# Performance work log

Measured on AMD Instinct MI355X. Metric: run time of the kernel, lower is better.

## Reference

```python
import jax, jax.numpy as jnp
import numpy as np

USER_NUM = 100000
ITEM_NUM = 200000
N_NODES = USER_NUM + ITEM_NUM
EMB_DIM = 64
NNZ = 2000000
BATCH = 4096
NODE_DROP = 0.1
MSG_DROP = 0.1
DECAY = 1e-4
NEG_SLOPE = 0.2
EPS = 1e-12


def setup_inputs() -> dict:
    key = jax.random.key(0)
    ks = jax.random.split(key, 24)
    inp = {
        'edge_row': jax.random.randint(ks[0], (NNZ,), 0, N_NODES, dtype=jnp.int32),
        'edge_col': jax.random.randint(ks[1], (NNZ,), 0, N_NODES, dtype=jnp.int32),
        'edge_vals': jax.random.uniform(ks[2], (NNZ,), dtype=jnp.float32),
        'user_emb': jax.random.normal(ks[3], (USER_NUM, EMB_DIM), dtype=jnp.float32) * 0.1,
        'item_emb': jax.random.normal(ks[4], (ITEM_NUM, EMB_DIM), dtype=jnp.float32) * 0.1,
        'user_id': jax.random.randint(ks[5], (BATCH,), 0, USER_NUM, dtype=jnp.int32),
        'item_id': jax.random.randint(ks[6], (BATCH,), 0, ITEM_NUM, dtype=jnp.int32),
        'neg_item_id': jax.random.randint(ks[7], (BATCH,), 0, ITEM_NUM, dtype=jnp.int32),
    }
    scale = 1.0 / np.sqrt(EMB_DIM)
    for k in range(3):
        inp['W_gc_%d' % k] = jax.random.normal(ks[8 + 4 * k], (EMB_DIM, EMB_DIM), dtype=jnp.float32) * scale
        inp['b_gc_%d' % k] = jax.random.normal(ks[9 + 4 * k], (1, EMB_DIM), dtype=jnp.float32) * 0.01
        inp['W_bi_%d' % k] = jax.random.normal(ks[10 + 4 * k], (EMB_DIM, EMB_DIM), dtype=jnp.float32) * scale
        inp['b_bi_%d' % k] = jax.random.normal(ks[11 + 4 * k], (1, EMB_DIM), dtype=jnp.float32) * 0.01
    return inp


def _ngcf_loss(edge_row, edge_col, edge_vals, user_emb, item_emb, layer_params,
               user_id, item_id, neg_item_id):
    # Deterministic dropout masks (fixed key) -> reproducible reference.
    key = jax.random.key(42)
    k_node, k_msg = jax.random.split(key)

    # Sparse (node) dropout on adjacency values, rescaled by 1/keep.
    keep_e = 1.0 - NODE_DROP
    emask = jax.random.bernoulli(k_node, keep_e, edge_vals.shape)
    vals = jnp.where(emask, edge_vals, 0.0) * (1.0 / keep_e)

    ego = jnp.concatenate([user_emb, item_emb], axis=0)  # [N, D]
    all_embs = [ego]
    keep_m = 1.0 - MSG_DROP
    for k, (Wg, bg, Wb, bb) in enumerate(layer_params):
        # SpMM: side[i] = sum_j A[i,j] * ego[j]  (irregular gather + segment_sum)
        gathered = vals[:, None] * ego[edge_col]          # [nnz, D]
        side = jax.ops.segment_sum(gathered, edge_row, num_segments=N_NODES)
        sum_emb = side @ Wg + bg                          # graph-conv transform
        bi_emb = (ego * side) @ Wb + bb                   # bi-interaction transform
        ego = jax.nn.leaky_relu(sum_emb + bi_emb, NEG_SLOPE)
        mmask = jax.random.bernoulli(jax.random.fold_in(k_msg, k), keep_m, ego.shape)
        ego = jnp.where(mmask, ego, 0.0) * (1.0 / keep_m)  # message dropout
        norm = jnp.sqrt(jnp.sum(ego * ego, axis=1, keepdims=True))
        all_embs.append(ego / jnp.maximum(norm, EPS))      # L2 normalize per node
    all_emb = jnp.concatenate(all_embs, axis=1)           # [N, 4*D]
    u_g = all_emb[:USER_NUM]
    i_g = all_emb[USER_NUM:]

    users = u_g[user_id]
    pos = i_g[item_id]
    neg = i_g[neg_item_id]
    pos_s = jnp.sum(users * pos, axis=1)
    neg_s = jnp.sum(users * neg, axis=1)
    mf_loss = -jnp.mean(jax.nn.log_sigmoid(pos_s - neg_s))
    reg = (jnp.sum(users ** 2) + jnp.sum(pos ** 2) + jnp.sum(neg ** 2)) * 0.5
    emb_loss = DECAY * reg / BATCH
    return mf_loss + emb_loss, mf_loss, emb_loss


def reference(edge_row, edge_col, edge_vals, user_emb, item_emb,
              W_gc_0, b_gc_0, W_bi_0, b_bi_0,
              W_gc_1, b_gc_1, W_bi_1, b_bi_1,
              W_gc_2, b_gc_2, W_bi_2, b_bi_2,
              user_id, item_id, neg_item_id):
    layer_params = [(W_gc_0, b_gc_0, W_bi_0, b_bi_0),
                    (W_gc_1, b_gc_1, W_bi_1, b_bi_1),
                    (W_gc_2, b_gc_2, W_bi_2, b_bi_2)]
    loss, mf_loss, emb_loss = _ngcf_loss(edge_row, edge_col, edge_vals,
                                         user_emb, item_emb, layer_params,
                                         user_id, item_id, neg_item_id)
    return loss, mf_loss, emb_loss
```

## Files before the change

kernel.cpp:

```cpp
#include <hip/hip_runtime.h>
#include <stdint.h>

#define USER_NUM 100000
#define ITEM_NUM 200000
#define N_NODES  300000
#define EMB      64
#define NNZ      2000000
#define BATCH    4096
#define R1M      1000000u
#define HALF_MSG 9600000u
#define HALF_N   150000
#define INVK     1.1111111111111112f

#define NBK2     256
#define BROWS    1172
#define BCAP2    7680
#define ABLK     480
#define ACH      4167
#define LDSCAP   3968

typedef short short8 __attribute__((ext_vector_type(8)));
typedef float f32x4  __attribute__((ext_vector_type(4)));

__host__ __device__ inline uint32_t rotl32(uint32_t v, int r) {
    return (v << r) | (v >> (32 - r));
}

__host__ __device__ inline void threefry2x32(uint32_t k0, uint32_t k1,
                                             uint32_t x0, uint32_t x1,
                                             uint32_t& o0, uint32_t& o1) {
    uint32_t k2 = k0 ^ k1 ^ 0x1BD11BDAu;
    x0 += k0; x1 += k1;
#define TF_R(r) { x0 += x1; x1 = rotl32(x1, r); x1 ^= x0; }
    TF_R(13) TF_R(15) TF_R(26) TF_R(6)
    x0 += k1; x1 += k2 + 1u;
    TF_R(17) TF_R(29) TF_R(16) TF_R(24)
    x0 += k2; x1 += k0 + 2u;
    TF_R(13) TF_R(15) TF_R(26) TF_R(6)
    x0 += k0; x1 += k1 + 3u;
    TF_R(17) TF_R(29) TF_R(16) TF_R(24)
    x0 += k1; x1 += k2 + 4u;
    TF_R(13) TF_R(15) TF_R(26) TF_R(6)
    x0 += k2; x1 += k0 + 5u;
#undef TF_R
    o0 = x0; o1 = x1;
}

__host__ __device__ inline float tf_uniform(uint32_t bits) {
    uint32_t fb = (bits >> 9) | 0x3f800000u;
    return __builtin_bit_cast(float, fb) - 1.0f;
}

__device__ inline float bf2f(uint16_t u) {
    uint32_t x = ((uint32_t)u) << 16;
    return __builtin_bit_cast(float, x);
}
__device__ inline uint16_t f2bf(float f) {
    uint32_t x = __builtin_bit_cast(uint32_t, f);
    uint32_t r = (x + 0x7FFFu + ((x >> 16) & 1u)) >> 16;
    return (uint16_t)r;
}

__global__ __launch_bounds__(256) void k_conv(const float* __restrict__ u,
                                              const float* __restrict__ it,
                                              uint16_t* __restrict__ dst) {
    int i = blockIdx.x * 256 + threadIdx.x;
    const int TOT = N_NODES * EMB / 4;
    if (i >= TOT) return;
    const int UQ = USER_NUM * EMB / 4;
    float4 f = (i < UQ) ? ((const float4*)u)[i] : ((const float4*)it)[i - UQ];
    ushort4 o;
    o.x = f2bf(f.x); o.y = f2bf(f.y); o.z = f2bf(f.z); o.w = f2bf(f.w);
    ((ushort4*)dst)[i] = o;
}

__global__ __launch_bounds__(256) void k_sortA(const int* __restrict__ erow,
                                               const int* __restrict__ ecol,
                                               const float* __restrict__ evals,
                                               uint32_t* __restrict__ bcnt,
                                               uint2* __restrict__ tmp,
                                               uint32_t kn0, uint32_t kn1) {
    __shared__ uint32_t hist[NBK2];
    __shared__ uint32_t lstart[NBK2];
    __shared__ uint32_t gbase[NBK2];
    __shared__ uint32_t cur[NBK2];
    __shared__ uint32_t eidx[LDSCAP];
    __shared__ uint8_t  keepb[ACH];
    int tid = threadIdx.x;
    int base = blockIdx.x * ACH;
    int lim = min(ACH, NNZ - base);
    hist[tid] = 0u;
    __syncthreads();
    for (int j = tid; j < lim; j += 256) {
        uint32_t e = (uint32_t)(base + j);
        uint32_t x0 = (e < R1M) ? e : e - R1M;
        uint32_t o0, o1;
        threefry2x32(kn0, kn1, x0, x0 + R1M, o0, o1);
        uint32_t bits = (e < R1M) ? o0 : o1;
        bool kp = tf_uniform(bits) < 0.9f;
        keepb[j] = kp ? 1u : 0u;
        if (kp) atomicAdd(&hist[(uint32_t)erow[e] / BROWS], 1u);
    }
    __syncthreads();
    uint32_t x = hist[tid];
    lstart[tid] = x;
    __syncthreads();
    for (int off = 1; off < 256; off <<= 1) {
        uint32_t y = (tid >= off) ? lstart[tid - off] : 0u;
        __syncthreads();
        lstart[tid] += y;
        __syncthreads();
    }
    uint32_t exc = lstart[tid] - x;
    uint32_t gb = 0u;
    if (x) gb = atomicAdd(&bcnt[tid], x);
    lstart[tid] = exc;
    gbase[tid] = gb;
    cur[tid] = exc;
    __syncthreads();
    for (int j = tid; j < lim; j += 256) {
        if (keepb[j]) {
            uint32_t e = (uint32_t)(base + j);
            uint32_t b = (uint32_t)erow[e] / BROWS;
            uint32_t p = atomicAdd(&cur[b], 1u);
            if (p < LDSCAP) eidx[p] = e;
        }
    }
    __syncthreads();
    uint32_t total = min(lstart[NBK2 - 1] + hist[NBK2 - 1], (uint32_t)LDSCAP);
    for (uint32_t p = tid; p < total; p += 256) {
        uint32_t e = eidx[p];
        uint32_t row = (uint32_t)erow[e];
        uint32_t b = row / BROWS;
        uint32_t off = gbase[b] + (p - lstart[b]);
        if (off < BCAP2) {
            uint2 q;
            q.x = (uint32_t)ecol[e] | ((row - b * BROWS) << 19);
            q.y = __builtin_bit_cast(uint32_t, evals[e] * INVK);
            tmp[(size_t)b * BCAP2 + off] = q;
        }
    }
}

__global__ __launch_bounds__(256) void k_sortB(const uint2* __restrict__ tmp,
                                               const uint32_t* __restrict__ bcnt,
                                               uint2* __restrict__ cv,
                                               uint32_t* __restrict__ rowstart,
                                               uint32_t* __restrict__ rowend) {
    __shared__ uint32_t hist[1280];
    __shared__ uint32_t tsum[256];
    int b = blockIdx.x;
    int t = threadIdx.x;
    uint32_t cnt = min(bcnt[b], (uint32_t)BCAP2);
    for (int i = t; i < 1280; i += 256) hist[i] = 0u;
    __syncthreads();
    const uint2* src = tmp + (size_t)b * BCAP2;
    for (uint32_t i = t; i < cnt; i += 256)
        atomicAdd(&hist[src[i].x >> 19], 1u);
    __syncthreads();
    uint32_t l[5];
    uint32_t s = 0u;
#pragma unroll
    for (int i = 0; i < 5; ++i) { l[i] = hist[t * 5 + i]; s += l[i]; }
    tsum[t] = s;
    __syncthreads();
    for (int off = 1; off < 256; off <<= 1) {
        uint32_t y = (t >= off) ? tsum[t - off] : 0u;
        __syncthreads();
        tsum[t] += y;
        __syncthreads();
    }
    uint32_t run = tsum[t] - s;
    uint32_t cvb = (uint32_t)b * BCAP2;
#pragma unroll
    for (int i = 0; i < 5; ++i) {
        uint32_t e0 = run;
        run += l[i];
        int idx = t * 5 + i;
        int row = b * BROWS + idx;
        if (idx < BROWS && row < N_NODES) {
            rowstart[row] = cvb + e0;
            rowend[row]   = cvb + run;
        }
        hist[idx] = e0;
    }
    __syncthreads();
    for (uint32_t i = t; i < cnt; i += 256) {
        uint2 p = src[i];
        uint32_t rl = p.x >> 19;
        uint32_t pos = atomicAdd(&hist[rl], 1u);
        uint2 q;
        q.x = p.x & 0x7FFFFu;
        q.y = p.y;
        cv[(size_t)cvb + pos] = q;
    }
}

__global__ __launch_bounds__(256) void k_spmv(const uint16_t* __restrict__ ego,
                                              uint16_t* __restrict__ side,
                                              const uint32_t* __restrict__ rowstart,
                                              const uint32_t* __restrict__ rowend,
                                              const uint2* __restrict__ cv) {
    int lane = threadIdx.x & 63;
    int wv = __builtin_amdgcn_readfirstlane((int)((blockIdx.x * 256 + threadIdx.x) >> 6));
    int nw = (gridDim.x * 256) >> 6;
    for (int n0 = wv * 2; n0 < N_NODES; n0 += nw * 2) {
        uint32_t st  = __builtin_amdgcn_readfirstlane(rowstart[n0]);
        uint32_t mid = __builtin_amdgcn_readfirstlane(rowend[n0]);
        uint32_t en  = __builtin_amdgcn_readfirstlane(rowend[n0 + 1]);
        float acc0 = 0.0f, acc1 = 0.0f;
        for (uint32_t j0 = st; j0 < en; j0 += 8) {
            uint32_t cx[8];
            float v0[8], v1[8];
#pragma unroll
            for (int u = 0; u < 8; ++u) {
                uint2 p = cv[j0 + u];
                uint32_t idx = j0 + (uint32_t)u;
                bool ok = idx < en;
                bool r1 = idx >= mid;
                cx[u] = ok ? p.x : 0u;
                float v = ok ? __builtin_bit_cast(float, p.y) : 0.0f;
                v0[u] = r1 ? 0.0f : v;
                v1[u] = r1 ? v : 0.0f;
            }
            float g[8];
#pragma unroll
            for (int u = 0; u < 8; ++u)
                g[u] = bf2f(ego[(size_t)cx[u] * 64 + lane]);
#pragma unroll
            for (int u = 0; u < 8; ++u) {
                acc0 = fmaf(v0[u], g[u], acc0);
                acc1 = fmaf(v1[u], g[u], acc1);
            }
        }
        side[(size_t)n0 * 64 + lane] = f2bf(acc0);
        side[(size_t)(n0 + 1) * 64 + lane] = f2bf(acc1);
    }
}

__device__ inline short8 mul_frag(short8 s, uint4 e) {
    uint32_t ew[4] = {e.x, e.y, e.z, e.w};
    short8 r;
#pragma unroll
    for (int i = 0; i < 4; ++i) {
        float a0 = bf2f((uint16_t)s[2 * i])     * bf2f((uint16_t)(ew[i] & 0xffffu));
        float a1 = bf2f((uint16_t)s[2 * i + 1]) * bf2f((uint16_t)(ew[i] >> 16));
        r[2 * i]     = (short)f2bf(a0);
        r[2 * i + 1] = (short)f2bf(a1);
    }
    return r;
}

__global__ __launch_bounds__(256) void k_dense_mfma(
        uint16_t* __restrict__ ego, const uint16_t* __restrict__ side,
        const float* __restrict__ Wg, const float* __restrict__ bg,
        const float* __restrict__ Wb, const float* __restrict__ bb,
        uint32_t km0, uint32_t km1) {
    int lane = threadIdx.x & 63;
    int wave = (blockIdx.x * 256 + threadIdx.x) >> 6;
    int nw = (gridDim.x * 256) >> 6;
    int m = lane & 15;
    int g = lane >> 4;

    short8 bfr[4][4];
#pragma unroll
    for (int kk = 0; kk < 4; ++kk) {
        const float* W = (kk < 2) ? Wg : Wb;
        int krow = (kk & 1) * 32 + 8 * g;
#pragma unroll
        for (int nt = 0; nt < 4; ++nt) {
#pragma unroll
            for (int i = 0; i < 8; ++i)
                bfr[kk][nt][i] = (short)f2bf(W[(krow + i) * 64 + 16 * nt + m]);
        }
    }
    float bias[4];
#pragma unroll
    for (int nt = 0; nt < 4; ++nt)
        bias[nt] = bg[16 * nt + m] + bb[16 * nt + m];

    for (int tile = wave; tile < HALF_N / 16; tile += nw) {
        int n0 = tile * 16;
        uint32_t keepB = 0;
        {
            const uint16_t* srow = side + (size_t)(n0 + m) * 64;
            const uint16_t* erw  = ego  + (size_t)(n0 + m) * 64;
            short8 a0 = *(const short8*)(srow + 8 * g);
            short8 a1 = *(const short8*)(srow + 32 + 8 * g);
            uint4  e0 = *(const uint4*)(erw + 8 * g);
            uint4  e1 = *(const uint4*)(erw + 32 + 8 * g);
            short8 a2 = mul_frag(a0, e0);
            short8 a3 = mul_frag(a1, e1);
            f32x4 acc[4];
#pragma unroll
            for (int nt = 0; nt < 4; ++nt) {
                acc[nt] = (f32x4)(0.0f);
                acc[nt] = __builtin_amdgcn_mfma_f32_16x16x32_bf16(a0, bfr[0][nt], acc[nt], 0, 0, 0);
                acc[nt] = __builtin_amdgcn_mfma_f32_16x16x32_bf16(a1, bfr[1][nt], acc[nt], 0, 0, 0);
                acc[nt] = __builtin_amdgcn_mfma_f32_16x16x32_bf16(a2, bfr[2][nt], acc[nt], 0, 0, 0);
                acc[nt] = __builtin_amdgcn_mfma_f32_16x16x32_bf16(a3, bfr[3][nt], acc[nt], 0, 0, 0);
            }
#pragma unroll
            for (int nt = 0; nt < 4; ++nt) {
#pragma unroll
                for (int i = 0; i < 4; ++i) {
                    int row = n0 + g * 4 + i;
                    int col = 16 * nt + m;
                    float h = acc[nt][i] + bias[nt];
                    h = (h >= 0.0f) ? h : 0.2f * h;
                    uint32_t j = (uint32_t)row * 64u + (uint32_t)col;
                    uint32_t o0, o1;
                    threefry2x32(km0, km1, j, j + HALF_MSG, o0, o1);
                    bool kA = tf_uniform(o0) < 0.9f;
                    keepB |= (uint32_t)(tf_uniform(o1) < 0.9f) << (nt * 4 + i);
                    ego[(size_t)row * 64 + col] = f2bf(kA ? h * INVK : 0.0f);
                }
            }
        }
        {
            int R = n0 + HALF_N;
            const uint16_t* srow = side + (size_t)(R + m) * 64;
            const uint16_t* erw  = ego  + (size_t)(R + m) * 64;
            short8 a0 = *(const short8*)(srow + 8 * g);
            short8 a1 = *(const short8*)(srow + 32 + 8 * g);
            uint4  e0 = *(const uint4*)(erw + 8 * g);
            uint4  e1 = *(const uint4*)(erw + 32 + 8 * g);
            short8 a2 = mul_frag(a0, e0);
            short8 a3 = mul_frag(a1, e1);
            f32x4 acc[4];
#pragma unroll
            for (int nt = 0; nt < 4; ++nt) {
                acc[nt] = (f32x4)(0.0f);
                acc[nt] = __builtin_amdgcn_mfma_f32_16x16x32_bf16(a0, bfr[0][nt], acc[nt], 0, 0, 0);
                acc[nt] = __builtin_amdgcn_mfma_f32_16x16x32_bf16(a1, bfr[1][nt], acc[nt], 0, 0, 0);
                acc[nt] = __builtin_amdgcn_mfma_f32_16x16x32_bf16(a2, bfr[2][nt], acc[nt], 0, 0, 0);
                acc[nt] = __builtin_amdgcn_mfma_f32_16x16x32_bf16(a3, bfr[3][nt], acc[nt], 0, 0, 0);
            }
#pragma unroll
            for (int nt = 0; nt < 4; ++nt) {
#pragma unroll
                for (int i = 0; i < 4; ++i) {
                    int row = R + g * 4 + i;
                    int col = 16 * nt + m;
                    float h = acc[nt][i] + bias[nt];
                    h = (h >= 0.0f) ? h : 0.2f * h;
                    bool kB = (keepB >> (nt * 4 + i)) & 1u;
                    ego[(size_t)row * 64 + col] = f2bf(kB ? h * INVK : 0.0f);
                }
            }
        }
    }
}

__device__ inline float wred64(float v) {
#pragma unroll
    for (int m = 32; m >= 1; m >>= 1) v += __shfl_xor(v, m, 64);
    return v;
}

__global__ __launch_bounds__(256) void k_segacc(const void* __restrict__ ua_,
                                                const void* __restrict__ ia_,
                                                const int* __restrict__ uid,
                                                const int* __restrict__ iid,
                                                const int* __restrict__ nid,
                                                float* __restrict__ dotp,
                                                float* __restrict__ dotn,
                                                float* __restrict__ sqs,
                                                int normalize, int f32) {
    int gt = blockIdx.x * 256 + threadIdx.x;
    int w = gt >> 6, lane = gt & 63;
    if (w >= BATCH) return;
    int u = uid[w], p = iid[w], n = nid[w];
    float eu, ep, en;
    if (f32) {
        const float* ua = (const float*)ua_;
        const float* ia = (const float*)ia_;
        eu = ua[(size_t)u * EMB + lane];
        ep = ia[(size_t)p * EMB + lane];
        en = ia[(size_t)n * EMB + lane];
    } else {
        const uint16_t* ua = (const uint16_t*)ua_;
        const uint16_t* ia = (const uint16_t*)ia_;
        eu = bf2f(ua[(size_t)u * EMB + lane]);
        ep = bf2f(ia[(size_t)p * EMB + lane]);
        en = bf2f(ia[(size_t)n * EMB + lane]);
    }
    if (normalize) {
        float su = wred64(eu * eu);
        float sp = wred64(ep * ep);
        float sn = wred64(en * en);
        eu /= fmaxf(sqrtf(su), 1e-12f);
        ep /= fmaxf(sqrtf(sp), 1e-12f);
        en /= fmaxf(sqrtf(sn), 1e-12f);
    }
    float dp = wred64(eu * ep);
    float dn = wred64(eu * en);
    float s3 = wred64(eu * eu + ep * ep + en * en);
    if (lane == 0) {
        dotp[w] += dp;
        dotn[w] += dn;
        sqs[w]  += s3;
    }
}

__global__ __launch_bounds__(256) void k_finalize(const float* __restrict__ dotp,
                                                  const float* __restrict__ dotn,
                                                  const float* __restrict__ sqs,
                                                  float* __restrict__ out) {
    __shared__ float smf[256], ssq[256];
    int t = threadIdx.x;
    float mf = 0.0f, s = 0.0f;
    for (int b = t; b < BATCH; b += 256) {
        float x = dotp[b] - dotn[b];
        float ls = fminf(x, 0.0f) - log1pf(expf(-fabsf(x)));
        mf += ls;
        s += sqs[b];
    }
    smf[t] = mf; ssq[t] = s;
    __syncthreads();
    for (int off = 128; off > 0; off >>= 1) {
        if (t < off) { smf[t] += smf[t + off]; ssq[t] += ssq[t + off]; }
        __syncthreads();
    }
    if (t == 0) {
        float mf_loss = -smf[0] / (float)BATCH;
        float reg = 0.5f * ssq[0];
        float emb_loss = (float)1e-4 * reg / (float)BATCH;
        out[0] = mf_loss + emb_loss;
        out[1] = mf_loss;
        out[2] = emb_loss;
    }
}

extern "C" void kernel_launch(void* const* d_in, const int* in_sizes, int n_in,
                              void* d_out, int out_size, void* d_ws, size_t ws_size,
                              hipStream_t stream) {
    const int*   erow  = (const int*)d_in[0];
    const int*   ecol  = (const int*)d_in[1];
    const float* evals = (const float*)d_in[2];
    const float* uemb  = (const float*)d_in[3];
    const float* iemb  = (const float*)d_in[4];
    const int*   uid   = (const int*)d_in[5];
    const int*   iid   = (const int*)d_in[6];
    const int*   nid   = (const int*)d_in[7];
    const float* Wg[3] = {(const float*)d_in[8],  (const float*)d_in[12], (const float*)d_in[16]};
    const float* bg[3] = {(const float*)d_in[9],  (const float*)d_in[13], (const float*)d_in[17]};
    const float* Wb[3] = {(const float*)d_in[10], (const float*)d_in[14], (const float*)d_in[18]};
    const float* bb[3] = {(const float*)d_in[11], (const float*)d_in[15], (const float*)d_in[19]};

    const size_t NBE = (size_t)NBK2 * BCAP2;
    uint2*    tmp      = (uint2*)d_ws;
    uint2*    cv       = tmp + NBE;
    uint16_t* side     = (uint16_t*)(cv + NBE + 8);
    uint16_t* ego      = side + (size_t)N_NODES * EMB;
    uint32_t* rowstart = (uint32_t*)(ego + (size_t)N_NODES * EMB);
    uint32_t* rowend   = rowstart + N_NODES;
    uint32_t* bcnt     = rowend + N_NODES;
    float*    dotp     = (float*)(bcnt + NBK2);
    float*    dotn     = dotp + BATCH;
    float*    sqs      = dotn + BATCH;
    size_t needed = (NBE * 2 + 8) * 8 + (size_t)N_NODES * EMB * 2 * 2
                  + ((size_t)2 * N_NODES + NBK2 + 3 * BATCH) * 4;
    if (ws_size < needed) return;

    uint32_t a0, b0, a1, b1;
    threefry2x32(0u, 42u, 0u, 2u, a0, b0);
    threefry2x32(0u, 42u, 1u, 3u, a1, b1);
    uint32_t knode0 = a0, knode1 = a1;
    uint32_t kmsg0  = b0, kmsg1  = b1;
    uint32_t mk[6];
    for (uint32_t k = 0; k < 3; ++k)
        threefry2x32(kmsg0, kmsg1, 0u, k, mk[2 * k], mk[2 * k + 1]);

    hipMemsetAsync(bcnt, 0, (size_t)NBK2 * 4, stream);
    hipMemsetAsync(dotp, 0, 3 * BATCH * 4, stream);

    k_conv<<<(N_NODES * EMB / 4 + 255) / 256, 256, 0, stream>>>(uemb, iemb, ego);
    k_sortA<<<ABLK, 256, 0, stream>>>(erow, ecol, evals, bcnt, tmp, knode0, knode1);
    k_sortB<<<NBK2, 256, 0, stream>>>(tmp, bcnt, cv, rowstart, rowend);

    k_segacc<<<BATCH * 64 / 256, 256, 0, stream>>>(uemb, iemb, uid, iid, nid,
                                                   dotp, dotn, sqs, 0, 1);

    for (int k = 0; k < 3; ++k) {
        k_spmv<<<2048, 256, 0, stream>>>(ego, side, rowstart, rowend, cv);
        k_dense_mfma<<<768, 256, 0, stream>>>(ego, side, Wg[k], bg[k], Wb[k], bb[k],
                                              mk[2 * k], mk[2 * k + 1]);
        k_segacc<<<BATCH * 64 / 256, 256, 0, stream>>>(ego, ego + (size_t)USER_NUM * EMB,
                                                       uid, iid, nid, dotp, dotn, sqs, 1, 0);
    }
    k_finalize<<<1, 256, 0, stream>>>(dotp, dotn, sqs, (float*)d_out);
}
```

Before: 470.6 us.

## Gather FP8 embedding copy in SpMM and pair threefry outputs in edge dropout

```diff
diff --git a/kernel.cpp b/kernel.cpp
--- a/kernel.cpp
+++ b/kernel.cpp
@@ -16,11 +16,17 @@
 #define BROWS    1172
 #define BCAP2    7680
 #define ABLK     480
-#define ACH      4167
+#define PCH      2084
 #define LDSCAP   3968
 
 typedef short short8 __attribute__((ext_vector_type(8)));
 typedef float f32x4  __attribute__((ext_vector_type(4)));
+
+#if defined(__has_builtin)
+# if __has_builtin(__builtin_amdgcn_cvt_f32_fp8)
+#  define HAS_CVT_FP8 1
+# endif
+#endif
 
 __host__ __device__ inline uint32_t rotl32(uint32_t v, int r) {
     return (v << r) | (v >> (32 - r));
@@ -61,9 +67,43 @@
     return (uint16_t)r;
 }
 
+__device__ inline float fp82f(uint32_t b) {
+#ifdef HAS_CVT_FP8
+    return __builtin_amdgcn_cvt_f32_fp8(b, 0);
+#else
+    uint32_t E = (b >> 3) & 15u, m = b & 7u;
+    float mag = E ? __builtin_bit_cast(float, ((E + 120u) << 23) | (m << 20))
+                  : (float)m * 0.001953125f;
+    return (b & 0x80u) ? -mag : mag;
+#endif
+}
+
+__device__ inline uint32_t f2fp8(float f) {
+    uint32_t u = __builtin_bit_cast(uint32_t, f);
+    uint32_t s = (u >> 31) << 7;
+    uint32_t a = u & 0x7fffffffu;
+    if (a >= 0x3C800000u) {
+        uint32_t m = a & 0x7fffffu;
+        uint32_t r = (m + 0x7FFFFu + ((m >> 20) & 1u)) >> 20;
+        uint32_t E = (a >> 23) - 120u;
+        if (r == 8u) { r = 0u; E += 1u; }
+        if (E > 15u || (E == 15u && r == 7u)) return s | 0x7Eu;
+        return s | (E << 3) | r;
+    }
+    if (a <= 0x3A800000u) return s;
+    uint32_t e8 = a >> 23;
+    uint32_t M = (a & 0x7fffffu) | 0x800000u;
+    int sh = 21 - ((int)e8 - 120);
+    uint32_t half = 1u << (sh - 1);
+    uint32_t m3 = (M + half - 1u + ((M >> sh) & 1u)) >> sh;
+    if (m3 >= 8u) return s | 0x08u;
+    return s | m3;
+}
+
 __global__ __launch_bounds__(256) void k_conv(const float* __restrict__ u,
                                               const float* __restrict__ it,
-                                              uint16_t* __restrict__ dst) {
+                                              uint16_t* __restrict__ dst,
+                                              uint8_t* __restrict__ dst8) {
     int i = blockIdx.x * 256 + threadIdx.x;
     const int TOT = N_NODES * EMB / 4;
     if (i >= TOT) return;
@@ -72,6 +112,8 @@
     ushort4 o;
     o.x = f2bf(f.x); o.y = f2bf(f.y); o.z = f2bf(f.z); o.w = f2bf(f.w);
     ((ushort4*)dst)[i] = o;
+    uint32_t p = f2fp8(f.x) | (f2fp8(f.y) << 8) | (f2fp8(f.z) << 16) | (f2fp8(f.w) << 24);
+    ((uint32_t*)dst8)[i] = p;
 }
 
 __global__ __launch_bounds__(256) void k_sortA(const int* __restrict__ erow,
@@ -85,21 +127,24 @@
     __shared__ uint32_t gbase[NBK2];
     __shared__ uint32_t cur[NBK2];
     __shared__ uint32_t eidx[LDSCAP];
-    __shared__ uint8_t  keepb[ACH];
+    __shared__ uint8_t  keepb[PCH];
     int tid = threadIdx.x;
-    int base = blockIdx.x * ACH;
-    int lim = min(ACH, NNZ - base);
+    uint32_t pbase = (uint32_t)blockIdx.x * PCH;
     hist[tid] = 0u;
     __syncthreads();
-    for (int j = tid; j < lim; j += 256) {
-        uint32_t e = (uint32_t)(base + j);
-        uint32_t x0 = (e < R1M) ? e : e - R1M;
-        uint32_t o0, o1;
-        threefry2x32(kn0, kn1, x0, x0 + R1M, o0, o1);
-        uint32_t bits = (e < R1M) ? o0 : o1;
-        bool kp = tf_uniform(bits) < 0.9f;
-        keepb[j] = kp ? 1u : 0u;
-        if (kp) atomicAdd(&hist[(uint32_t)erow[e] / BROWS], 1u);
+    for (int j = tid; j < PCH; j += 256) {
+        uint32_t t = pbase + (uint32_t)j;
+        uint8_t kb = 0u;
+        if (t < R1M) {
+            uint32_t o0, o1;
+            threefry2x32(kn0, kn1, t, t + R1M, o0, o1);
+            bool k0 = tf_uniform(o0) < 0.9f;
+            bool k1 = tf_uniform(o1) < 0.9f;
+            kb = (uint8_t)((k0 ? 1u : 0u) | (k1 ? 2u : 0u));
+            if (k0) atomicAdd(&hist[(uint32_t)erow[t] / BROWS], 1u);
+            if (k1) atomicAdd(&hist[(uint32_t)erow[t + R1M] / BROWS], 1u);
+        }
+        keepb[j] = kb;
     }
     __syncthreads();
     uint32_t x = hist[tid];
@@ -118,12 +163,20 @@
     gbase[tid] = gb;
     cur[tid] = exc;
     __syncthreads();
-    for (int j = tid; j < lim; j += 256) {
-        if (keepb[j]) {
-            uint32_t e = (uint32_t)(base + j);
-            uint32_t b = (uint32_t)erow[e] / BROWS;
+    for (int j = tid; j < PCH; j += 256) {
+        uint8_t kb = keepb[j];
+        if (!kb) continue;
+        uint32_t t = pbase + (uint32_t)j;
+        if (kb & 1u) {
+            uint32_t b = (uint32_t)erow[t] / BROWS;
             uint32_t p = atomicAdd(&cur[b], 1u);
-            if (p < LDSCAP) eidx[p] = e;
+            if (p < LDSCAP) eidx[p] = t;
+        }
+        if (kb & 2u) {
+            uint32_t e2 = t + R1M;
+            uint32_t b = (uint32_t)erow[e2] / BROWS;
+            uint32_t p = atomicAdd(&cur[b], 1u);
+            if (p < LDSCAP) eidx[p] = e2;
         }
     }
     __syncthreads();
@@ -196,7 +249,7 @@
     }
 }
 
-__global__ __launch_bounds__(256) void k_spmv(const uint16_t* __restrict__ ego,
+__global__ __launch_bounds__(256) void k_spmv(const uint8_t* __restrict__ ego8,
                                               uint16_t* __restrict__ side,
                                               const uint32_t* __restrict__ rowstart,
                                               const uint32_t* __restrict__ rowend,
@@ -226,7 +279,7 @@
             float g[8];
 #pragma unroll
             for (int u = 0; u < 8; ++u)
-                g[u] = bf2f(ego[(size_t)cx[u] * 64 + lane]);
+                g[u] = fp82f((uint32_t)ego8[(size_t)cx[u] * 64u + (uint32_t)lane]);
 #pragma unroll
             for (int u = 0; u < 8; ++u) {
                 acc0 = fmaf(v0[u], g[u], acc0);
@@ -252,7 +305,8 @@
 }
 
 __global__ __launch_bounds__(256) void k_dense_mfma(
-        uint16_t* __restrict__ ego, const uint16_t* __restrict__ side,
+        uint16_t* __restrict__ ego, uint8_t* __restrict__ ego8,
+        const uint16_t* __restrict__ side,
         const float* __restrict__ Wg, const float* __restrict__ bg,
         const float* __restrict__ Wb, const float* __restrict__ bb,
         uint32_t km0, uint32_t km1) {
@@ -313,7 +367,9 @@
                     threefry2x32(km0, km1, j, j + HALF_MSG, o0, o1);
                     bool kA = tf_uniform(o0) < 0.9f;
                     keepB |= (uint32_t)(tf_uniform(o1) < 0.9f) << (nt * 4 + i);
-                    ego[(size_t)row * 64 + col] = f2bf(kA ? h * INVK : 0.0f);
+                    float val = kA ? h * INVK : 0.0f;
+                    ego[(size_t)row * 64 + col] = f2bf(val);
+                    ego8[(size_t)row * 64 + col] = (uint8_t)f2fp8(val);
                 }
             }
         }
@@ -345,7 +401,9 @@
                     float h = acc[nt][i] + bias[nt];
                     h = (h >= 0.0f) ? h : 0.2f * h;
                     bool kB = (keepB >> (nt * 4 + i)) & 1u;
-                    ego[(size_t)row * 64 + col] = f2bf(kB ? h * INVK : 0.0f);
+                    float val = kB ? h * INVK : 0.0f;
+                    ego[(size_t)row * 64 + col] = f2bf(val);
+                    ego8[(size_t)row * 64 + col] = (uint8_t)f2fp8(val);
                 }
             }
         }
@@ -453,13 +511,14 @@
     uint2*    cv       = tmp + NBE;
     uint16_t* side     = (uint16_t*)(cv + NBE + 8);
     uint16_t* ego      = side + (size_t)N_NODES * EMB;
-    uint32_t* rowstart = (uint32_t*)(ego + (size_t)N_NODES * EMB);
+    uint8_t*  ego8     = (uint8_t*)(ego + (size_t)N_NODES * EMB);
+    uint32_t* rowstart = (uint32_t*)(ego8 + (size_t)N_NODES * EMB);
     uint32_t* rowend   = rowstart + N_NODES;
     uint32_t* bcnt     = rowend + N_NODES;
     float*    dotp     = (float*)(bcnt + NBK2);
     float*    dotn     = dotp + BATCH;
     float*    sqs      = dotn + BATCH;
-    size_t needed = (NBE * 2 + 8) * 8 + (size_t)N_NODES * EMB * 2 * 2
+    size_t needed = (NBE * 2 + 8) * 8 + (size_t)N_NODES * EMB * (2 * 2 + 1)
                   + ((size_t)2 * N_NODES + NBK2 + 3 * BATCH) * 4;
     if (ws_size < needed) return;
 
@@ -475,7 +534,7 @@
     hipMemsetAsync(bcnt, 0, (size_t)NBK2 * 4, stream);
     hipMemsetAsync(dotp, 0, 3 * BATCH * 4, stream);
 
-    k_conv<<<(N_NODES * EMB / 4 + 255) / 256, 256, 0, stream>>>(uemb, iemb, ego);
+    k_conv<<<(N_NODES * EMB / 4 + 255) / 256, 256, 0, stream>>>(uemb, iemb, ego, ego8);
     k_sortA<<<ABLK, 256, 0, stream>>>(erow, ecol, evals, bcnt, tmp, knode0, knode1);
     k_sortB<<<NBK2, 256, 0, stream>>>(tmp, bcnt, cv, rowstart, rowend);
 
@@ -483,8 +542,8 @@
                                                    dotp, dotn, sqs, 0, 1);
 
     for (int k = 0; k < 3; ++k) {
-        k_spmv<<<2048, 256, 0, stream>>>(ego, side, rowstart, rowend, cv);
-        k_dense_mfma<<<768, 256, 0, stream>>>(ego, side, Wg[k], bg[k], Wb[k], bb[k],
+        k_spmv<<<2048, 256, 0, stream>>>(ego8, side, rowstart, rowend, cv);
+        k_dense_mfma<<<768, 256, 0, stream>>>(ego, ego8, side, Wg[k], bg[k], Wb[k], bb[k],
                                               mk[2 * k], mk[2 * k + 1]);
         k_segacc<<<BATCH * 64 / 256, 256, 0, stream>>>(ego, ego + (size_t)USER_NUM * EMB,
                                                        uid, iid, nid, dotp, dotn, sqs, 1, 0);
```

After: 526.4 us. +11.8%, slower.
